# Performance work log

Hardware: AMD Instinct MI355X
Metric: run time of the kernel (lower is better)

The kernel has to match this reference:

```python
import jax, jax.numpy as jnp
import numpy as np

NUM_ROUTED = 256
DIM = 2048
TOPK = 8
ROUTE_SCALE = 2.5


def setup_inputs() -> dict:
    key = jax.random.key(0)
    k_x, k_w = jax.random.split(key)
    x = jax.random.normal(k_x, (4, 4096, DIM), dtype=jnp.float32)
    # nn.Parameter(torch.empty) -> treat as learned weight; init small normal
    weight = jax.random.normal(k_w, (NUM_ROUTED, DIM), dtype=jnp.float32) * 0.02
    bias = jnp.zeros((NUM_ROUTED,), dtype=jnp.float32)
    return {"x": x, "weight": weight, "bias": bias}


def reference(x, weight, bias):
    # logits: [b, s, e]
    logits = jnp.einsum("bsd,ed->bse", x, weight)
    scores = jax.nn.sigmoid(logits)
    scores_for_selection = scores + bias  # bias only affects selection
    _, indices = jax.lax.top_k(scores_for_selection, TOPK)  # [b, s, k]
    weights = jnp.take_along_axis(scores, indices, axis=-1)  # gather original scores
    weights = weights / (jnp.sum(weights, axis=-1, keepdims=True) + 1e-20)
    weights = weights * ROUTE_SCALE
    return weights, indices
```

## Files before the change

### kernel.cpp

```cpp
#include <hip/hip_runtime.h>
#include <math.h>
#include <limits.h>

#define DIM 2048
#define NEXP 256
#define TOPK 8
#define BM 16
#define BK 16
#define NTH 256
#define NTILE 128


typedef float f32x2 __attribute__((ext_vector_type(2)));

__device__ __forceinline__ f32x2 pkmul(f32x2 a, f32x2 b) {
    f32x2 d;
    asm("v_pk_mul_f32 %0, %1, %2" : "=v"(d) : "v"(a), "v"(b));
    return d;
}
__device__ __forceinline__ f32x2 pkadd(f32x2 a, f32x2 b) {
    f32x2 d;
    asm("v_pk_add_f32 %0, %1, %2" : "=v"(d) : "v"(a), "v"(b));
    return d;
}

__device__ __forceinline__ void gload16(const void* gptr, void* lptr) {
    __builtin_amdgcn_global_load_lds(
        (const __attribute__((address_space(1))) unsigned int*)(unsigned long long)gptr,
        (__attribute__((address_space(3))) unsigned int*)(unsigned int)(unsigned long long)lptr,
        16, 0, 0);
}

__global__ __launch_bounds__(NTH) void gate_kernel(
    const float* __restrict__ x, const float* __restrict__ w,
    const float* __restrict__ bias, float* __restrict__ outw,
    float* __restrict__ outi)
{
#pragma clang fp contract(off)
    __shared__ float wbuf[2][4096];
    __shared__ float xbuf[2][256];

    const int tid   = threadIdx.x;
    const int elane = tid & 63;
    const int r0    = (tid >> 6) * 4;
    const int gr    = blockIdx.x * BM;

    const char* wbase = (const char*)w + (size_t)tid * (DIM * 4);
    const int xrow = tid >> 2, xq = tid & 3;
    const char* xbase = (const char*)x + ((size_t)(gr + xrow) * DIM + xq * 4) * 4;

    auto stage = [&](int buf, int kt) {
        const size_t kb = (size_t)kt * 64;
        char* dst = (char*)&wbuf[buf][0] + tid * 16;
        gload16(wbase + kb,      dst);
        gload16(wbase + kb + 16, dst + 4096);
        gload16(wbase + kb + 32, dst + 8192);
        gload16(wbase + kb + 48, dst + 12288);
        if (tid < 64)
            gload16(xbase + kb, (char*)&xbuf[buf][0] + tid * 16);
    };

    f32x2 acc[4][4][2];
#pragma unroll
    for (int r = 0; r < 4; ++r)
#pragma unroll
        for (int i = 0; i < 4; ++i)
#pragma unroll
            for (int p = 0; p < 2; ++p) acc[r][i][p] = (f32x2){0.0f, 0.0f};

    auto compute = [&](int buf) {
#pragma unroll
        for (int c = 3; c >= 0; --c) {
            f32x2 xlo[4], xhi[4];
#pragma unroll
            for (int r = 0; r < 4; ++r) {
                const float4 xv = *(const float4*)&xbuf[buf][(r0 + r) * BK + c * 4];
                xlo[r] = (f32x2){xv.x, xv.y};
                xhi[r] = (f32x2){xv.z, xv.w};
            }
            __builtin_amdgcn_s_setprio(1);
#pragma unroll
            for (int i = 0; i < 4; ++i) {
                const float4 wv = *(const float4*)&wbuf[buf][(c * 256 + elane + 64 * i) * 4];
                const f32x2 wlo = (f32x2){wv.x, wv.y};
                const f32x2 whi = (f32x2){wv.z, wv.w};
#pragma unroll
                for (int r = 0; r < 4; ++r) {
                    acc[r][i][0] = pkadd(acc[r][i][0], pkmul(xlo[r], wlo));
                    acc[r][i][1] = pkadd(acc[r][i][1], pkmul(xhi[r], whi));
                }
            }
            __builtin_amdgcn_s_setprio(0);
        }
    };

    stage(0, 0);
    __syncthreads();
    for (int kt = 0; kt < NTILE; ++kt) {
        const int buf = kt & 1;
        if (kt + 1 < NTILE) stage(buf ^ 1, kt + 1);
        compute(buf);
        __syncthreads();
    }

    float* sc = &wbuf[0][0];
#pragma unroll
    for (int r = 0; r < 4; ++r)
#pragma unroll
        for (int i = 0; i < 4; ++i) {
            const float l01 = acc[r][i][0].x + acc[r][i][0].y;
            const float l23 = acc[r][i][1].x + acc[r][i][1].y;
            const float logit = l01 + l23;
            const double s = 1.0 / (1.0 + exp(-(double)logit));
            sc[(r0 + r) * NEXP + (elane + 64 * i)] = (float)s;
        }
    __syncthreads();

    float* cval = &wbuf[1][0];
    int*   cidx = (int*)&wbuf[1][1024];

    if (tid < 128) {
        const int row = tid >> 3;
        const int sub = tid & 7;
        float tv[TOPK];
        int   ti[TOPK];
#pragma unroll
        for (int q = 0; q < TOPK; ++q) { tv[q] = -INFINITY; ti[q] = INT_MAX; }
        for (int j = 0; j < 32; ++j) {
            const int e = sub + (j << 3);
            const float v = sc[row * NEXP + e] + bias[e];
            if (v > tv[TOPK - 1]) {
                int p = TOPK - 1;
                while (p > 0 && v > tv[p - 1]) {
                    tv[p] = tv[p - 1]; ti[p] = ti[p - 1]; --p;
                }
                tv[p] = v; ti[p] = e;
            }
        }
#pragma unroll
        for (int q = 0; q < TOPK; ++q) {
            cval[row * 64 + sub * 8 + q] = tv[q];
            cidx[row * 64 + sub * 8 + q] = ti[q];
        }
    }
    __syncthreads();

    if (tid < 128 && (tid & 7) == 0) {
        const int row = tid >> 3;
        int p[8];
#pragma unroll
        for (int s = 0; s < 8; ++s) p[s] = 0;
        float g[TOPK];
        int   sel[TOPK];
        for (int k = 0; k < TOPK; ++k) {
            float best = -INFINITY;
            int bidx = INT_MAX;
            int bs = 0;
            for (int s = 0; s < 8; ++s) {
                if (p[s] < 8) {
                    const float v = cval[row * 64 + s * 8 + p[s]];
                    const int  id = cidx[row * 64 + s * 8 + p[s]];
                    if (v > best || (v == best && id < bidx)) {
                        best = v; bidx = id; bs = s;
                    }
                }
            }
            p[bs]++;
            sel[k] = bidx;
            g[k] = sc[row * NEXP + bidx];
        }
        const float s01 = g[0] + g[1], s23 = g[2] + g[3];
        const float s45 = g[4] + g[5], s67 = g[6] + g[7];
        const float wsum = (s01 + s23) + (s45 + s67);
        const float den = wsum + 1e-20f;
        const size_t orow = (size_t)(gr + row) * TOPK;
#pragma unroll
        for (int k = 0; k < TOPK; ++k) {
            outw[orow + k] = (g[k] / den) * 2.5f;
            outi[orow + k] = (float)sel[k];
        }
    }
}

extern "C" void kernel_launch(void* const* d_in, const int* in_sizes, int n_in,
                              void* d_out, int out_size, void* d_ws, size_t ws_size,
                              hipStream_t stream) {
    const float* x    = (const float*)d_in[0];
    const float* w    = (const float*)d_in[1];
    const float* bias = (const float*)d_in[2];
    float* outw = (float*)d_out;
    const int M = in_sizes[0] / DIM;
    float* outi = outw + (size_t)M * TOPK;
    const int grid = M / BM;
    hipLaunchKernelGGL(gate_kernel, dim3(grid), dim3(NTH), 0, stream,
                       x, w, bias, outw, outi);
}
```

Measured before the change: 414.3 us.

## Double rows per block with 512 threads and reduce top-k merge to two-way

Each block now handles 32 token rows with 512 threads. The two thread halves split the per-tile weight staging, so every weight tile fetched into LDS is reused across twice as many rows and total weight traffic per token is halved. The top-k stage is reorganized: 64 threads each scan 128 experts, then one thread per row does a two-way merge, and the candidate buffers move into the freed x buffer. The cost is a longer serial scan per thread in the top-k phase and a larger block, which may change occupancy.

```diff
diff --git a/kernel.cpp b/kernel.cpp
--- a/kernel.cpp
+++ b/kernel.cpp
@@ -5,9 +5,9 @@
 #define DIM 2048
 #define NEXP 256
 #define TOPK 8
-#define BM 16
+#define BM 32
 #define BK 16
-#define NTH 256
+#define NTH 512
 #define NTILE 128
 
 
@@ -38,25 +38,26 @@
 {
 #pragma clang fp contract(off)
     __shared__ float wbuf[2][4096];
-    __shared__ float xbuf[2][256];
+    __shared__ float xbuf[2][512];
 
     const int tid   = threadIdx.x;
     const int elane = tid & 63;
     const int r0    = (tid >> 6) * 4;
     const int gr    = blockIdx.x * BM;
 
-    const char* wbase = (const char*)w + (size_t)tid * (DIM * 4);
+    const int we    = tid & 255;
+    const int chalf = tid >> 8;
+    const char* wbase = (const char*)w + (size_t)we * (DIM * 4);
     const int xrow = tid >> 2, xq = tid & 3;
     const char* xbase = (const char*)x + ((size_t)(gr + xrow) * DIM + xq * 4) * 4;
 
     auto stage = [&](int buf, int kt) {
         const size_t kb = (size_t)kt * 64;
-        char* dst = (char*)&wbuf[buf][0] + tid * 16;
-        gload16(wbase + kb,      dst);
-        gload16(wbase + kb + 16, dst + 4096);
-        gload16(wbase + kb + 32, dst + 8192);
-        gload16(wbase + kb + 48, dst + 12288);
-        if (tid < 64)
+        char* dst = (char*)&wbuf[buf][0] + we * 16;
+        const int c0 = chalf * 2;
+        gload16(wbase + kb + c0 * 16,        dst + c0 * 4096);
+        gload16(wbase + kb + (c0 + 1) * 16,  dst + (c0 + 1) * 4096);
+        if (tid < 128)
             gload16(xbase + kb, (char*)&xbuf[buf][0] + tid * 16);
     };
 
@@ -116,18 +117,18 @@
         }
     __syncthreads();
 
-    float* cval = &wbuf[1][0];
-    int*   cidx = (int*)&wbuf[1][1024];
+    float* cval = &xbuf[0][0];
+    int*   cidx = (int*)&xbuf[1][0];
 
-    if (tid < 128) {
-        const int row = tid >> 3;
-        const int sub = tid & 7;
+    if (tid < 64) {
+        const int row = tid >> 1;
+        const int sub = tid & 1;
         float tv[TOPK];
         int   ti[TOPK];
 #pragma unroll
         for (int q = 0; q < TOPK; ++q) { tv[q] = -INFINITY; ti[q] = INT_MAX; }
-        for (int j = 0; j < 32; ++j) {
-            const int e = sub + (j << 3);
+        for (int j = 0; j < 128; ++j) {
+            const int e = sub + (j << 1);
             const float v = sc[row * NEXP + e] + bias[e];
             if (v > tv[TOPK - 1]) {
                 int p = TOPK - 1;
@@ -139,35 +140,31 @@
         }
 #pragma unroll
         for (int q = 0; q < TOPK; ++q) {
-            cval[row * 64 + sub * 8 + q] = tv[q];
-            cidx[row * 64 + sub * 8 + q] = ti[q];
+            cval[row * 16 + sub * 8 + q] = tv[q];
+            cidx[row * 16 + sub * 8 + q] = ti[q];
         }
     }
     __syncthreads();
 
-    if (tid < 128 && (tid & 7) == 0) {
-        const int row = tid >> 3;
-        int p[8];
-#pragma unroll
-        for (int s = 0; s < 8; ++s) p[s] = 0;
+    if (tid < 32) {
+        const int row = tid;
+        int p0 = 0, p1 = 0;
         float g[TOPK];
         int   sel[TOPK];
+#pragma unroll
         for (int k = 0; k < TOPK; ++k) {
-            float best = -INFINITY;
-            int bidx = INT_MAX;
-            int bs = 0;
-            for (int s = 0; s < 8; ++s) {
-                if (p[s] < 8) {
-                    const float v = cval[row * 64 + s * 8 + p[s]];
-                    const int  id = cidx[row * 64 + s * 8 + p[s]];
-                    if (v > best || (v == best && id < bidx)) {
-                        best = v; bidx = id; bs = s;
-                    }
-                }
-            }
-            p[bs]++;
-            sel[k] = bidx;
-            g[k] = sc[row * NEXP + bidx];
+            const float v0 = cval[row * 16 + p0];
+            const int   i0 = cidx[row * 16 + p0];
+            const float v1 = cval[row * 16 + 8 + p1];
+            const int   i1 = cidx[row * 16 + 8 + p1];
+            int take0;
+            if (v0 > v1) take0 = 1;
+            else if (v1 > v0) take0 = 0;
+            else take0 = (i0 < i1);
+            const int e = take0 ? i0 : i1;
+            p0 += take0; p1 += 1 - take0;
+            sel[k] = e;
+            g[k] = sc[row * NEXP + e];
         }
         const float s01 = g[0] + g[1], s23 = g[2] + g[3];
         const float s45 = g[4] + g[5], s67 = g[6] + g[7];
```

Result: faster. 395.3 us (-4.6%).

## Single-buffer LDS staging and restructure top-k selection to 4 sub-lists per row

Applied to the files above, without the earlier changes.

Drops double buffering of the weight and x tiles in LDS, halving shared memory so more blocks can be resident per CU. It now stages, syncs, computes and syncs each iteration, so loads are no longer overlapped with compute inside a block. Latency hiding must instead come from other resident blocks. The top-k phase also changes from 8 to 4 partial lists per row, with a dedicated candidate buffer and an unrolled merge.

```diff
diff --git a/kernel.cpp b/kernel.cpp
--- a/kernel.cpp
+++ b/kernel.cpp
@@ -37,8 +37,10 @@
     float* __restrict__ outi)
 {
 #pragma clang fp contract(off)
-    __shared__ float wbuf[2][4096];
-    __shared__ float xbuf[2][256];
+    __shared__ float wbuf[4096];
+    __shared__ float xbuf[256];
+    __shared__ float cval[16 * 32];
+    __shared__ int   cidx[16 * 32];
 
     const int tid   = threadIdx.x;
     const int elane = tid & 63;
@@ -49,15 +51,15 @@
     const int xrow = tid >> 2, xq = tid & 3;
     const char* xbase = (const char*)x + ((size_t)(gr + xrow) * DIM + xq * 4) * 4;
 
-    auto stage = [&](int buf, int kt) {
+    auto stage = [&](int kt) {
         const size_t kb = (size_t)kt * 64;
-        char* dst = (char*)&wbuf[buf][0] + tid * 16;
+        char* dst = (char*)&wbuf[0] + tid * 16;
         gload16(wbase + kb,      dst);
         gload16(wbase + kb + 16, dst + 4096);
         gload16(wbase + kb + 32, dst + 8192);
         gload16(wbase + kb + 48, dst + 12288);
         if (tid < 64)
-            gload16(xbase + kb, (char*)&xbuf[buf][0] + tid * 16);
+            gload16(xbase + kb, (char*)&xbuf[0] + tid * 16);
     };
 
     f32x2 acc[4][4][2];
@@ -68,20 +70,20 @@
 #pragma unroll
             for (int p = 0; p < 2; ++p) acc[r][i][p] = (f32x2){0.0f, 0.0f};
 
-    auto compute = [&](int buf) {
+    auto compute = [&]() {
 #pragma unroll
         for (int c = 3; c >= 0; --c) {
             f32x2 xlo[4], xhi[4];
 #pragma unroll
             for (int r = 0; r < 4; ++r) {
-                const float4 xv = *(const float4*)&xbuf[buf][(r0 + r) * BK + c * 4];
+                const float4 xv = *(const float4*)&xbuf[(r0 + r) * BK + c * 4];
                 xlo[r] = (f32x2){xv.x, xv.y};
                 xhi[r] = (f32x2){xv.z, xv.w};
             }
             __builtin_amdgcn_s_setprio(1);
 #pragma unroll
             for (int i = 0; i < 4; ++i) {
-                const float4 wv = *(const float4*)&wbuf[buf][(c * 256 + elane + 64 * i) * 4];
+                const float4 wv = *(const float4*)&wbuf[(c * 256 + elane + 64 * i) * 4];
                 const f32x2 wlo = (f32x2){wv.x, wv.y};
                 const f32x2 whi = (f32x2){wv.z, wv.w};
 #pragma unroll
@@ -94,16 +96,14 @@
         }
     };
 
-    stage(0, 0);
-    __syncthreads();
     for (int kt = 0; kt < NTILE; ++kt) {
-        const int buf = kt & 1;
-        if (kt + 1 < NTILE) stage(buf ^ 1, kt + 1);
-        compute(buf);
+        stage(kt);
+        __syncthreads();
+        compute();
         __syncthreads();
     }
 
-    float* sc = &wbuf[0][0];
+    float* sc = &wbuf[0];
 #pragma unroll
     for (int r = 0; r < 4; ++r)
 #pragma unroll
@@ -116,18 +116,15 @@
         }
     __syncthreads();
 
-    float* cval = &wbuf[1][0];
-    int*   cidx = (int*)&wbuf[1][1024];
-
-    if (tid < 128) {
-        const int row = tid >> 3;
-        const int sub = tid & 7;
+    if (tid < 64) {
+        const int row = tid >> 2;
+        const int sub = tid & 3;
         float tv[TOPK];
         int   ti[TOPK];
 #pragma unroll
         for (int q = 0; q < TOPK; ++q) { tv[q] = -INFINITY; ti[q] = INT_MAX; }
-        for (int j = 0; j < 32; ++j) {
-            const int e = sub + (j << 3);
+        for (int j = 0; j < 64; ++j) {
+            const int e = sub + (j << 2);
             const float v = sc[row * NEXP + e] + bias[e];
             if (v > tv[TOPK - 1]) {
                 int p = TOPK - 1;
@@ -139,27 +136,28 @@
         }
 #pragma unroll
         for (int q = 0; q < TOPK; ++q) {
-            cval[row * 64 + sub * 8 + q] = tv[q];
-            cidx[row * 64 + sub * 8 + q] = ti[q];
+            cval[row * 32 + sub * 8 + q] = tv[q];
+            cidx[row * 32 + sub * 8 + q] = ti[q];
         }
     }
     __syncthreads();
 
-    if (tid < 128 && (tid & 7) == 0) {
-        const int row = tid >> 3;
-        int p[8];
+    if (tid < 16) {
+        const int row = tid;
+        int p[4];
 #pragma unroll
-        for (int s = 0; s < 8; ++s) p[s] = 0;
+        for (int s = 0; s < 4; ++s) p[s] = 0;
         float g[TOPK];
         int   sel[TOPK];
         for (int k = 0; k < TOPK; ++k) {
             float best = -INFINITY;
             int bidx = INT_MAX;
             int bs = 0;
-            for (int s = 0; s < 8; ++s) {
+#pragma unroll
+            for (int s = 0; s < 4; ++s) {
                 if (p[s] < 8) {
-                    const float v = cval[row * 64 + s * 8 + p[s]];
-                    const int  id = cidx[row * 64 + s * 8 + p[s]];
+                    const float v = cval[row * 32 + s * 8 + p[s]];
+                    const int  id = cidx[row * 32 + s * 8 + p[s]];
                     if (v > best || (v == best && id < bidx)) {
                         best = v; bidx = id; bs = s;
                     }
```

Result: slower. 444.5 us (+7.3%).
